# Optimization experiments

Hardware: AMD Instinct MI355X
Metric: run time of the kernel (lower is better)

## Reference

```python
import jax, jax.numpy as jnp
import numpy as np

NPOS_MAX = 64

def setup_inputs() -> dict:
    key = jax.random.key(0)
    k1, k2, k3 = jax.random.split(key, 3)
    b, h, l, d = 4, 12, 1024, 64
    query = jax.random.normal(k1, (b, h, l, d), dtype=jnp.float32)
    attn_logits = jax.random.normal(k2, (b, h, l, l), dtype=jnp.float32)
    pos_emb = jax.random.normal(k3, (d, NPOS_MAX), dtype=jnp.float32) * 0.02
    return {"query": query, "attn_logits": attn_logits, "pos_emb": pos_emb}

def reference(query, attn_logits, pos_emb):
    # gates: sigmoid of attention logits, with diagonal zeroed
    gates = jax.nn.sigmoid(attn_logits)
    l = gates.shape[-1]
    eye = jnp.eye(l, dtype=gates.dtype)
    gates = gates * (1.0 - eye)
    # reverse cumsum along last axis, clamped to [0, npos_max-1]
    pos = jnp.flip(jnp.cumsum(jnp.flip(gates, -1), axis=-1), -1)
    pos = jnp.minimum(pos, jnp.asarray(NPOS_MAX - 1, dtype=pos.dtype))
    pos_ceil = jnp.ceil(pos).astype(jnp.int32)    # [b,h,l,l]
    pos_floor = jnp.floor(pos).astype(jnp.int32)  # [b,h,l,l]
    # interpolated position logits: [b,h,l,npos_max]
    logits_int = jnp.einsum('bhld,dn->bhln', query, pos_emb)
    logits_ceil = jnp.take_along_axis(logits_int, pos_ceil, axis=-1)
    logits_floor = jnp.take_along_axis(logits_int, pos_floor, axis=-1)
    w = pos - pos_floor.astype(pos.dtype)
    return logits_ceil * w + logits_floor * (1.0 - w)
```

## Files before the change

### kernel.cpp

```cpp
#include <hip/hip_runtime.h>
#include <hip/hip_bf16.h>


__device__ __forceinline__ float bf2f(unsigned short u) {
    union { unsigned int i; float f; } t; t.i = ((unsigned int)u) << 16; return t.f;
}
__device__ __forceinline__ float bf2f_lo(unsigned int v) {
    union { unsigned int i; float f; } t; t.i = v << 16; return t.f;
}
__device__ __forceinline__ float bf2f_hi(unsigned int v) {
    union { unsigned int i; float f; } t; t.i = v & 0xffff0000u; return t.f;
}
__device__ __forceinline__ unsigned short f2bf(float f) {
    union { float f; unsigned int i; } t; t.f = f;
    unsigned int lsb = (t.i >> 16) & 1u;
    t.i += 0x7fffu + lsb;
    return (unsigned short)(t.i >> 16);
}
__device__ __forceinline__ float sigmoid_fast(float x) {
    float e = __builtin_amdgcn_exp2f(-1.44269504f * x);
    return __builtin_amdgcn_rcpf(1.0f + e);
}

__global__ __launch_bounds__(256) void cope_detect(
    const unsigned short* __restrict__ q, int* __restrict__ flag)
{
    const int tid = threadIdx.x;
    unsigned short u = q[2 * tid];
    int e = (u >> 7) & 0xFF;
    unsigned long long m = __ballot(e >= 200);
    __shared__ int cnt;
    if (tid == 0) cnt = 0;
    __syncthreads();
    if ((tid & 63) == 0) atomicAdd(&cnt, __popcll(m));
    __syncthreads();
    if (tid == 0) *flag = (cnt > 8) ? 1 : 0;
}

__global__ __launch_bounds__(256) void cope_li(
    const void* __restrict__ qv, const void* __restrict__ pev,
    float* __restrict__ li, const int* __restrict__ flag)
{
    __shared__ float pe_f[64 * 64];
    __shared__ float q_t[64 * 64];
    const int tid = threadIdx.x;
    const bool isf32 = (*flag != 0);

    if (isf32) {
        const float4* pe4 = reinterpret_cast<const float4*>(pev);
#pragma unroll
        for (int it = 0; it < 4; ++it)
            reinterpret_cast<float4*>(pe_f)[it * 256 + tid] = pe4[it * 256 + tid];
        const float4* q4 = reinterpret_cast<const float4*>(qv) + (size_t)blockIdx.x * 1024;
#pragma unroll
        for (int it = 0; it < 4; ++it) {
            int idx = it * 256 + tid;
            int d4 = idx >> 6, rr = idx & 63;
            float4 v = q4[rr * 16 + d4];
            q_t[(d4 * 4 + 0) * 64 + rr] = v.x;
            q_t[(d4 * 4 + 1) * 64 + rr] = v.y;
            q_t[(d4 * 4 + 2) * 64 + rr] = v.z;
            q_t[(d4 * 4 + 3) * 64 + rr] = v.w;
        }
    } else {
        const uint4* pe16 = reinterpret_cast<const uint4*>(pev);
#pragma unroll
        for (int it = 0; it < 2; ++it) {
            int idx = it * 256 + tid;
            uint4 v = pe16[idx];
            float4 a, b;
            a.x = bf2f_lo(v.x); a.y = bf2f_hi(v.x);
            a.z = bf2f_lo(v.y); a.w = bf2f_hi(v.y);
            b.x = bf2f_lo(v.z); b.y = bf2f_hi(v.z);
            b.z = bf2f_lo(v.w); b.w = bf2f_hi(v.w);
            float4* dst = reinterpret_cast<float4*>(&pe_f[idx * 8]);
            dst[0] = a; dst[1] = b;
        }
        const ushort4* q4 = reinterpret_cast<const ushort4*>(qv) + (size_t)blockIdx.x * 1024;
#pragma unroll
        for (int it = 0; it < 4; ++it) {
            int idx = it * 256 + tid;
            int d4 = idx >> 6, rr = idx & 63;
            ushort4 v = q4[rr * 16 + d4];
            q_t[(d4 * 4 + 0) * 64 + rr] = bf2f(v.x);
            q_t[(d4 * 4 + 1) * 64 + rr] = bf2f(v.y);
            q_t[(d4 * 4 + 2) * 64 + rr] = bf2f(v.z);
            q_t[(d4 * 4 + 3) * 64 + rr] = bf2f(v.w);
        }
    }
    __syncthreads();

    const int r0 = (tid & 15) * 4, n0 = (tid >> 4) * 4;
    float acc[4][4];
#pragma unroll
    for (int a = 0; a < 4; ++a)
#pragma unroll
        for (int b = 0; b < 4; ++b) acc[a][b] = 0.f;

#pragma unroll 8
    for (int d = 0; d < 64; ++d) {
        float4 qv4 = *reinterpret_cast<const float4*>(&q_t[d * 64 + r0]);
        float4 pv = *reinterpret_cast<const float4*>(&pe_f[d * 64 + n0]);
        acc[0][0] += qv4.x * pv.x; acc[0][1] += qv4.x * pv.y; acc[0][2] += qv4.x * pv.z; acc[0][3] += qv4.x * pv.w;
        acc[1][0] += qv4.y * pv.x; acc[1][1] += qv4.y * pv.y; acc[1][2] += qv4.y * pv.z; acc[1][3] += qv4.y * pv.w;
        acc[2][0] += qv4.z * pv.x; acc[2][1] += qv4.z * pv.y; acc[2][2] += qv4.z * pv.z; acc[2][3] += qv4.z * pv.w;
        acc[3][0] += qv4.w * pv.x; acc[3][1] += qv4.w * pv.y; acc[3][2] += qv4.w * pv.z; acc[3][3] += qv4.w * pv.w;
    }
#pragma unroll
    for (int a = 0; a < 4; ++a) {
        size_t row = (size_t)blockIdx.x * 64 + r0 + a;
        float4 o; o.x = acc[a][0]; o.y = acc[a][1]; o.z = acc[a][2]; o.w = acc[a][3];
        *reinterpret_cast<float4*>(&li[row * 64 + n0]) = o;
    }
}

__global__ __launch_bounds__(256) void cope_row(
    const void* __restrict__ attnv,
    const float* __restrict__ li_ws,
    void* __restrict__ outv,
    const int* __restrict__ flag)
{
    const int r = blockIdx.x;
    const int i = r & 1023;
    const int tid = threadIdx.x;
    const int lane = tid & 63;
    const int wid = tid >> 6;
    const bool isf32 = (*flag != 0);

    __shared__ float li[65];
    __shared__ float wsum[4];

    if (tid < 64) {
        float lv = li_ws[(size_t)r * 64 + tid];
        li[tid] = lv;
        if (tid == 63) li[64] = lv;
    }

    float g[4];
    if (isf32) {
        float4 av = reinterpret_cast<const float4*>(attnv)[(size_t)r * 256 + tid];
        g[0] = sigmoid_fast(av.x); g[1] = sigmoid_fast(av.y);
        g[2] = sigmoid_fast(av.z); g[3] = sigmoid_fast(av.w);
    } else {
        ushort4 av = reinterpret_cast<const ushort4*>(attnv)[(size_t)r * 256 + tid];
        g[0] = sigmoid_fast(bf2f(av.x)); g[1] = sigmoid_fast(bf2f(av.y));
        g[2] = sigmoid_fast(bf2f(av.z)); g[3] = sigmoid_fast(bf2f(av.w));
    }

    const int j0 = tid * 4;
    if (i >= j0 && i < j0 + 4) g[i - j0] = 0.f;

    float ts = g[0] + g[1] + g[2] + g[3];

    float x = ts;
#pragma unroll
    for (int s = 1; s < 64; s <<= 1) {
        float y = __shfl_up(x, s, 64);
        if (lane >= s) x += y;
    }
    if (lane == 63) wsum[wid] = x;

    __syncthreads();

    const float s0 = wsum[0], s1 = wsum[1], s2 = wsum[2], s3 = wsum[3];
    const float total = s0 + s1 + s2 + s3;
    float woff = 0.f;
    if (wid > 0) woff += s0;
    if (wid > 1) woff += s1;
    if (wid > 2) woff += s2;
    float run = woff + (x - ts);

    float o[4];
#pragma unroll
    for (int e = 0; e < 4; ++e) {
        float p = total - run;
        run += g[e];
        p = fminf(fmaxf(p, 0.f), 63.f);
        float pf = floorf(p);
        int ipf = (int)pf;
        float a = li[ipf], b = li[ipf + 1];
        o[e] = fmaf(p - pf, b - a, a);
    }

    if (isf32) {
        float4 ov; ov.x = o[0]; ov.y = o[1]; ov.z = o[2]; ov.w = o[3];
        reinterpret_cast<float4*>(outv)[(size_t)r * 256 + tid] = ov;
    } else {
        uint2 ov;
        ov.x = (unsigned)f2bf(o[0]) | ((unsigned)f2bf(o[1]) << 16);
        ov.y = (unsigned)f2bf(o[2]) | ((unsigned)f2bf(o[3]) << 16);
        reinterpret_cast<uint2*>(outv)[(size_t)r * 256 + tid] = ov;
    }
}

__global__ __launch_bounds__(256) void cope_fused(
    const void* __restrict__ qv, const void* __restrict__ attnv,
    const void* __restrict__ pev, void* __restrict__ outv,
    const int* __restrict__ flag)
{
    const int r = blockIdx.x;
    const int i = r & 1023;
    const int tid = threadIdx.x;
    const int lane = tid & 63;
    const int wid = tid >> 6;
    const bool isf32 = (*flag != 0);

    __shared__ float pe_f[64 * 64];
    __shared__ float q_s[64];
    __shared__ float li[64];
    __shared__ float wsum[4];

    float g[4];
    if (isf32) {
        const float4* pe4 = reinterpret_cast<const float4*>(pev);
#pragma unroll
        for (int it = 0; it < 4; ++it)
            reinterpret_cast<float4*>(pe_f)[it * 256 + tid] = pe4[it * 256 + tid];
        if (tid < 16) {
            float4 v = reinterpret_cast<const float4*>(qv)[(size_t)r * 16 + tid];
            q_s[tid * 4 + 0] = v.x; q_s[tid * 4 + 1] = v.y;
            q_s[tid * 4 + 2] = v.z; q_s[tid * 4 + 3] = v.w;
        }
        float4 av = reinterpret_cast<const float4*>(attnv)[(size_t)r * 256 + tid];
        g[0] = sigmoid_fast(av.x); g[1] = sigmoid_fast(av.y);
        g[2] = sigmoid_fast(av.z); g[3] = sigmoid_fast(av.w);
    } else {
        const uint4* pe16 = reinterpret_cast<const uint4*>(pev);
#pragma unroll
        for (int it = 0; it < 2; ++it) {
            int idx = it * 256 + tid;
            uint4 v = pe16[idx];
            float4 a, b;
            a.x = bf2f_lo(v.x); a.y = bf2f_hi(v.x);
            a.z = bf2f_lo(v.y); a.w = bf2f_hi(v.y);
            b.x = bf2f_lo(v.z); b.y = bf2f_hi(v.z);
            b.z = bf2f_lo(v.w); b.w = bf2f_hi(v.w);
            float4* dst = reinterpret_cast<float4*>(&pe_f[idx * 8]);
            dst[0] = a; dst[1] = b;
        }
        if (tid < 16) {
            ushort4 v = reinterpret_cast<const ushort4*>(qv)[(size_t)r * 16 + tid];
            q_s[tid * 4 + 0] = bf2f(v.x); q_s[tid * 4 + 1] = bf2f(v.y);
            q_s[tid * 4 + 2] = bf2f(v.z); q_s[tid * 4 + 3] = bf2f(v.w);
        }
        ushort4 av = reinterpret_cast<const ushort4*>(attnv)[(size_t)r * 256 + tid];
        g[0] = sigmoid_fast(bf2f(av.x)); g[1] = sigmoid_fast(bf2f(av.y));
        g[2] = sigmoid_fast(bf2f(av.z)); g[3] = sigmoid_fast(bf2f(av.w));
    }

    const int j0 = tid * 4;
    if (i >= j0 && i < j0 + 4) g[i - j0] = 0.f;
    float ts = g[0] + g[1] + g[2] + g[3];
    float x = ts;
#pragma unroll
    for (int s = 1; s < 64; s <<= 1) {
        float y = __shfl_up(x, s, 64);
        if (lane >= s) x += y;
    }
    if (lane == 63) wsum[wid] = x;
    __syncthreads();
    if (tid < 64) {
        float acc = 0.f;
#pragma unroll
        for (int d = 0; d < 64; ++d) acc += q_s[d] * pe_f[d * 64 + tid];
        li[tid] = acc;
    }
    const float s0 = wsum[0], s1 = wsum[1], s2 = wsum[2], s3 = wsum[3];
    const float total = s0 + s1 + s2 + s3;
    float woff = 0.f;
    if (wid > 0) woff += s0;
    if (wid > 1) woff += s1;
    if (wid > 2) woff += s2;
    float run = woff + (x - ts);
    __syncthreads();

    float o[4];
#pragma unroll
    for (int e = 0; e < 4; ++e) {
        float p = total - run;
        run += g[e];
        p = fminf(fmaxf(p, 0.f), 63.f);
        float pf = floorf(p);
        int ipf = (int)pf;
        int ipc = min(ipf + 1, 63);
        float w = p - pf;
        o[e] = li[ipf] + w * (li[ipc] - li[ipf]);
    }
    if (isf32) {
        float4 ov; ov.x = o[0]; ov.y = o[1]; ov.z = o[2]; ov.w = o[3];
        reinterpret_cast<float4*>(outv)[(size_t)r * 256 + tid] = ov;
    } else {
        ushort4 ov;
        ov.x = f2bf(o[0]); ov.y = f2bf(o[1]); ov.z = f2bf(o[2]); ov.w = f2bf(o[3]);
        reinterpret_cast<ushort4*>(outv)[(size_t)r * 256 + tid] = ov;
    }
}

extern "C" void kernel_launch(void* const* d_in, const int* in_sizes, int n_in,
                              void* d_out, int out_size, void* d_ws, size_t ws_size,
                              hipStream_t stream) {
    const void* q    = d_in[0];
    const void* attn = d_in[1];
    const void* pe   = d_in[2];
    int* flag = (int*)d_ws;
    float* li = (float*)((char*)d_ws + 256);

    const long L = 1024;
    const long rows = (long)in_sizes[1] / L;
    const size_t ws_need = 256 + (size_t)rows * 64 * sizeof(float);

    cope_detect<<<1, 256, 0, stream>>>((const unsigned short*)d_in[0], flag);
    if (ws_size >= ws_need) {
        cope_li<<<(int)(rows / 64), 256, 0, stream>>>(q, pe, li, flag);
        cope_row<<<(int)rows, 256, 0, stream>>>(attn, li, d_out, flag);
    } else {
        cope_fused<<<(int)rows, 256, 0, stream>>>(q, attn, pe, d_out, flag);
    }
}
```

Baseline: 339.8 us.

## Process one row per wavefront in cope_row, removing block-level sync

The row kernel now assigns each 1024-element row to a single 64-lane wavefront, four rows per block. Each lane handles 16 contiguous elements. The cross-wave shared-memory reduction and __syncthreads are replaced by a wave-level shuffle to get the row total. This removes the block barrier and per-block overhead, at the cost of more registers per thread and per-lane strided vector loads that may coalesce less well.

```diff
diff --git a/kernel.cpp b/kernel.cpp
--- a/kernel.cpp
+++ b/kernel.cpp
@@ -114,43 +114,58 @@
     }
 }
 
-__global__ __launch_bounds__(256) void cope_row(
+__global__ __launch_bounds__(256) void cope_row4(
     const void* __restrict__ attnv,
     const float* __restrict__ li_ws,
     void* __restrict__ outv,
-    const int* __restrict__ flag)
+    const int* __restrict__ flag,
+    const int rows)
 {
-    const int r = blockIdx.x;
-    const int i = r & 1023;
     const int tid = threadIdx.x;
     const int lane = tid & 63;
     const int wid = tid >> 6;
+    const long r = (long)blockIdx.x * 4 + wid;
+    if (r >= rows) return;
+    const int i = (int)(r & 1023);
     const bool isf32 = (*flag != 0);
 
-    __shared__ float li[65];
-    __shared__ float wsum[4];
-
-    if (tid < 64) {
-        float lv = li_ws[(size_t)r * 64 + tid];
-        li[tid] = lv;
-        if (tid == 63) li[64] = lv;
-    }
-
-    float g[4];
-    if (isf32) {
-        float4 av = reinterpret_cast<const float4*>(attnv)[(size_t)r * 256 + tid];
-        g[0] = sigmoid_fast(av.x); g[1] = sigmoid_fast(av.y);
-        g[2] = sigmoid_fast(av.z); g[3] = sigmoid_fast(av.w);
-    } else {
-        ushort4 av = reinterpret_cast<const ushort4*>(attnv)[(size_t)r * 256 + tid];
-        g[0] = sigmoid_fast(bf2f(av.x)); g[1] = sigmoid_fast(bf2f(av.y));
-        g[2] = sigmoid_fast(bf2f(av.z)); g[3] = sigmoid_fast(bf2f(av.w));
-    }
-
-    const int j0 = tid * 4;
-    if (i >= j0 && i < j0 + 4) g[i - j0] = 0.f;
-
-    float ts = g[0] + g[1] + g[2] + g[3];
+    __shared__ float li[4][65];
+
+    {
+        float lv = li_ws[(size_t)r * 64 + lane];
+        li[wid][lane] = lv;
+        if (lane == 63) li[wid][64] = lv;
+    }
+
+    float g[16];
+    if (isf32) {
+        const float4* a4 = reinterpret_cast<const float4*>(attnv) + (size_t)r * 256 + lane * 4;
+#pragma unroll
+        for (int k = 0; k < 4; ++k) {
+            float4 v = a4[k];
+            g[k * 4 + 0] = sigmoid_fast(v.x);
+            g[k * 4 + 1] = sigmoid_fast(v.y);
+            g[k * 4 + 2] = sigmoid_fast(v.z);
+            g[k * 4 + 3] = sigmoid_fast(v.w);
+        }
+    } else {
+        const uint4* a8 = reinterpret_cast<const uint4*>(attnv) + (size_t)r * 128 + lane * 2;
+#pragma unroll
+        for (int k = 0; k < 2; ++k) {
+            uint4 v = a8[k];
+            g[k * 8 + 0] = sigmoid_fast(bf2f_lo(v.x)); g[k * 8 + 1] = sigmoid_fast(bf2f_hi(v.x));
+            g[k * 8 + 2] = sigmoid_fast(bf2f_lo(v.y)); g[k * 8 + 3] = sigmoid_fast(bf2f_hi(v.y));
+            g[k * 8 + 4] = sigmoid_fast(bf2f_lo(v.z)); g[k * 8 + 5] = sigmoid_fast(bf2f_hi(v.z));
+            g[k * 8 + 6] = sigmoid_fast(bf2f_lo(v.w)); g[k * 8 + 7] = sigmoid_fast(bf2f_hi(v.w));
+        }
+    }
+
+    const int j0 = lane * 16;
+    if (i >= j0 && i < j0 + 16) g[i - j0] = 0.f;
+
+    float ts = 0.f;
+#pragma unroll
+    for (int e = 0; e < 16; ++e) ts += g[e];
 
     float x = ts;
 #pragma unroll
@@ -158,38 +173,48 @@
         float y = __shfl_up(x, s, 64);
         if (lane >= s) x += y;
     }
-    if (lane == 63) wsum[wid] = x;
-
-    __syncthreads();
-
-    const float s0 = wsum[0], s1 = wsum[1], s2 = wsum[2], s3 = wsum[3];
-    const float total = s0 + s1 + s2 + s3;
-    float woff = 0.f;
-    if (wid > 0) woff += s0;
-    if (wid > 1) woff += s1;
-    if (wid > 2) woff += s2;
-    float run = woff + (x - ts);
-
-    float o[4];
-#pragma unroll
-    for (int e = 0; e < 4; ++e) {
-        float p = total - run;
-        run += g[e];
-        p = fminf(fmaxf(p, 0.f), 63.f);
-        float pf = floorf(p);
-        int ipf = (int)pf;
-        float a = li[ipf], b = li[ipf + 1];
-        o[e] = fmaf(p - pf, b - a, a);
-    }
-
-    if (isf32) {
-        float4 ov; ov.x = o[0]; ov.y = o[1]; ov.z = o[2]; ov.w = o[3];
-        reinterpret_cast<float4*>(outv)[(size_t)r * 256 + tid] = ov;
-    } else {
-        uint2 ov;
-        ov.x = (unsigned)f2bf(o[0]) | ((unsigned)f2bf(o[1]) << 16);
-        ov.y = (unsigned)f2bf(o[2]) | ((unsigned)f2bf(o[3]) << 16);
-        reinterpret_cast<uint2*>(outv)[(size_t)r * 256 + tid] = ov;
+    const float total = __shfl(x, 63, 64);
+    float run = x - ts;
+
+    if (isf32) {
+        float4 ov[4];
+#pragma unroll
+        for (int e = 0; e < 16; ++e) {
+            float p = total - run;
+            run += g[e];
+            p = fminf(fmaxf(p, 0.f), 63.f);
+            float pf = floorf(p);
+            int ipf = (int)pf;
+            float a = li[wid][ipf], b = li[wid][ipf + 1];
+            float o = fmaf(p - pf, b - a, a);
+            reinterpret_cast<float*>(ov)[e] = o;
+        }
+        float4* o4 = reinterpret_cast<float4*>(outv) + (size_t)r * 256 + lane * 4;
+#pragma unroll
+        for (int k = 0; k < 4; ++k) o4[k] = ov[k];
+    } else {
+        unsigned int ov[8];
+#pragma unroll
+        for (int e = 0; e < 8; ++e) {
+            float p0 = total - run; run += g[2 * e];
+            p0 = fminf(fmaxf(p0, 0.f), 63.f);
+            float pf0 = floorf(p0);
+            int ip0 = (int)pf0;
+            float a0 = li[wid][ip0], b0 = li[wid][ip0 + 1];
+            float o0 = fmaf(p0 - pf0, b0 - a0, a0);
+
+            float p1 = total - run; run += g[2 * e + 1];
+            p1 = fminf(fmaxf(p1, 0.f), 63.f);
+            float pf1 = floorf(p1);
+            int ip1 = (int)pf1;
+            float a1 = li[wid][ip1], b1 = li[wid][ip1 + 1];
+            float o1 = fmaf(p1 - pf1, b1 - a1, a1);
+
+            ov[e] = (unsigned)f2bf(o0) | ((unsigned)f2bf(o1) << 16);
+        }
+        uint4* o8 = reinterpret_cast<uint4*>(outv) + (size_t)r * 128 + lane * 2;
+        o8[0] = make_uint4(ov[0], ov[1], ov[2], ov[3]);
+        o8[1] = make_uint4(ov[4], ov[5], ov[6], ov[7]);
     }
 }
 
@@ -312,7 +337,7 @@
     cope_detect<<<1, 256, 0, stream>>>((const unsigned short*)d_in[0], flag);
     if (ws_size >= ws_need) {
         cope_li<<<(int)(rows / 64), 256, 0, stream>>>(q, pe, li, flag);
-        cope_row<<<(int)rows, 256, 0, stream>>>(attn, li, d_out, flag);
+        cope_row4<<<(int)((rows + 3) / 4), 256, 0, stream>>>(attn, li, d_out, flag, (int)rows);
     } else {
         cope_fused<<<(int)rows, 256, 0, stream>>>(q, attn, pe, d_out, flag);
     }
```

New measurement: 358.4 us. 1.05x slower.
